# Kernel optimization log

Measured on AMD Instinct MI355X. Metric: run time of the kernel, lower is better.

## Reference

```python
import jax, jax.numpy as jnp
import numpy as np

NHEAD = 12
EPS = 1e-5


def layernorm_nobias(x, gamma):
    mu = jnp.mean(x, axis=-1, keepdims=True)
    var = jnp.var(x, axis=-1, keepdims=True)
    return (x - mu) * jax.lax.rsqrt(var + EPS) * gamma


def setup_inputs() -> dict:
    key = jax.random.key(0)
    ks = jax.random.split(key, 10)
    b, l, d = 4, 2048, 768
    s = d ** -0.5
    return {
        "x": jax.random.normal(ks[0], (b, l, d), jnp.float32),
        "Wq": jax.random.normal(ks[1], (d, d), jnp.float32) * s,
        "Wk": jax.random.normal(ks[2], (d, d), jnp.float32) * s,
        "bk": jax.random.normal(ks[3], (d,), jnp.float32) * 0.02,
        "Wv": jax.random.normal(ks[4], (d, d), jnp.float32) * s,
        "bv": jax.random.normal(ks[5], (d,), jnp.float32) * 0.02,
        "gq": jnp.ones((d,), jnp.float32),
        "gk": jnp.ones((d,), jnp.float32),
        "Wo": jax.random.normal(ks[6], (d, d), jnp.float32) * s,
        "bo": jnp.zeros((d,), jnp.float32),
    }


def reference(x, Wq, Wk, bk, Wv, bv, gq, gk, Wo, bo):
    b, l, d = x.shape
    n = NHEAD
    hd = d // n
    scale = hd ** -0.5
    # projections (torch Linear: x @ W.T + b), QK-norm over full dmodel
    q = layernorm_nobias(x @ Wq.T, gq)
    k = layernorm_nobias(x @ Wk.T + bk, gk)
    v = x @ Wv.T + bv
    # split heads: b l (n hd) -> b n l hd
    q = q.reshape(b, l, n, hd).transpose(0, 2, 1, 3)
    k = k.reshape(b, l, n, hd).transpose(0, 2, 1, 3)
    v = v.reshape(b, l, n, hd).transpose(0, 2, 1, 3)
    # scores [b, n, l_q, l_k]; NOTE: softmax over the QUERY axis (dim=-2)
    scores = jnp.einsum('bnqd,bnkd->bnqk', q, k) * scale
    attn = jax.nn.softmax(scores, axis=-2)
    o = jnp.einsum('bnqk,bnkd->bnqd', attn, v)
    o = o.transpose(0, 2, 1, 3).reshape(b, l, d)
    return o @ Wo.T + bo + x
```

## Files before the change

kernel.cpp:

```cpp
#include <hip/hip_runtime.h>
#include <cstddef>
#include <cstdint>


typedef unsigned short u16;
typedef short  bf16x8 __attribute__((ext_vector_type(8)));
typedef float  f32x4  __attribute__((ext_vector_type(4)));
typedef unsigned short u16x8 __attribute__((ext_vector_type(8)));
typedef unsigned short u16x4 __attribute__((ext_vector_type(4)));

#define B_   4
#define L_   2048
#define D_   768
#define NH_  12
#define HD_  64
#define M_   (B_*L_)
#define SC2  (0.125f * 1.44269504088896f)

__device__ __forceinline__ float ex2(float x) { return __builtin_amdgcn_exp2f(x); }

__device__ __forceinline__ u16 f2bf(float f) {
    union { float f; unsigned u; } v; v.f = f;
    unsigned r = v.u + 0x7FFFu + ((v.u >> 16) & 1u);
    return (u16)(r >> 16);
}
__device__ __forceinline__ float bf2f(u16 b) {
    union { unsigned u; float f; } v; v.u = ((unsigned)b) << 16;
    return v.f;
}
__device__ __forceinline__ unsigned fbits(float f) {
    union { float f; unsigned u; } v; v.f = f; return v.u;
}
__device__ __forceinline__ unsigned packbf(float lo, float hi) {
    return __builtin_amdgcn_perm(fbits(hi), fbits(lo), 0x07060302u);
}

__device__ __forceinline__ void gld16(const void* g, void* l) {
    __builtin_amdgcn_global_load_lds(
        (const __attribute__((address_space(1))) unsigned*)g,
        (__attribute__((address_space(3))) unsigned*)l, 16, 0, 0);
}

__global__ __launch_bounds__(256) void cvt_all(
    const float* __restrict__ X,
    const float* __restrict__ W0, const float* __restrict__ W1,
    const float* __restrict__ W2, const float* __restrict__ W3,
    u16* __restrict__ Yx,
    u16* __restrict__ Y0, u16* __restrict__ Y1,
    u16* __restrict__ Y2, u16* __restrict__ Y3)
{
    const int nX8 = (M_ * D_) / 8;
    const int nW8 = (D_ * D_) / 8;
    int i = blockIdx.x * 256 + threadIdx.x;
    if (i >= nX8 + 4 * nW8) return;
    const float* S; u16* Dst; int off;
    if (i < nX8) { S = X; Dst = Yx; off = i; }
    else {
        int j = i - nX8;
        int w = j / nW8; off = j - w * nW8;
        S   = (w == 0) ? W0 : (w == 1) ? W1 : (w == 2) ? W2 : W3;
        Dst = (w == 0) ? Y0 : (w == 1) ? Y1 : (w == 2) ? Y2 : Y3;
    }
    const float4* xp = (const float4*)S + (size_t)off * 2;
    float4 a = xp[0], b = xp[1];
    u16x8 o;
    o[0] = f2bf(a.x); o[1] = f2bf(a.y); o[2] = f2bf(a.z); o[3] = f2bf(a.w);
    o[4] = f2bf(b.x); o[5] = f2bf(b.y); o[6] = f2bf(b.z); o[7] = f2bf(b.w);
    *((u16x8*)Dst + off) = o;
}

__global__ __launch_bounds__(256, 4) void gemm_qkv(
    const u16* __restrict__ A,
    const u16* __restrict__ W0, const u16* __restrict__ W1,
    const u16* __restrict__ W2,
    const float* __restrict__ bk, const float* __restrict__ bv,
    u16* __restrict__ q_o, u16* __restrict__ k_o, u16* __restrict__ v_o)
{
    __shared__ __align__(16) u16 lds[16384];
    __shared__ float bs[128];
    const int tid  = threadIdx.x;
    const int lane = tid & 63, w = tid >> 6;
    const int s    = lane & 15, quad = lane >> 4;
    const int bid  = blockIdx.x;
    const int xcd  = bid & 7, j0 = bid >> 3;
    const int bm   = (xcd * 8 + j0 / 18) * 128;
    const int sub  = j0 % 18;
    const int seg  = sub / 6;
    const int bn   = (sub % 6) * 128;
    const u16* W = (seg == 0) ? W0 : ((seg == 1) ? W1 : W2);
    u16* OUT = (seg == 0) ? q_o : ((seg == 1) ? k_o : v_o);
    const int mh = (w >> 1) * 64, nh = (w & 1) * 64;
    const int wb = tid & ~63;
    const int cq = quad ^ ((s >> 1) & 3);

    if (tid < 128)
        bs[tid] = (seg == 1) ? bk[bn + tid] : ((seg == 2) ? bv[bn + tid] : 0.0f);

    f32x4 acc[4][4];
    #pragma unroll
    for (int j = 0; j < 4; ++j)
        #pragma unroll
        for (int i = 0; i < 4; ++i) acc[j][i] = (f32x4){0.f, 0.f, 0.f, 0.f};

    {
        int c = tid, r = c >> 2, cs = (c & 3) ^ ((r >> 1) & 3);
        gld16(A + (size_t)(bm + r) * D_ + cs * 8, lds + (size_t)wb * 8);
        gld16(W + (size_t)(bn + r) * D_ + cs * 8, lds + 8192 + (size_t)wb * 8);
        c = tid + 256; r = c >> 2; cs = (c & 3) ^ ((r >> 1) & 3);
        gld16(A + (size_t)(bm + r) * D_ + cs * 8, lds + (size_t)(wb + 256) * 8);
        gld16(W + (size_t)(bn + r) * D_ + cs * 8, lds + 8192 + (size_t)(wb + 256) * 8);
    }
    __syncthreads();

    for (int t = 0; t < 24; ++t) {
        const u16* Ab = lds + (t & 1) * 4096;
        const u16* Bb = lds + 8192 + (t & 1) * 4096;
        if (t < 23) {
            const int k0 = (t + 1) * 32;
            u16* Ad = lds + ((t + 1) & 1) * 4096;
            u16* Bd = lds + 8192 + ((t + 1) & 1) * 4096;
            int c = tid, r = c >> 2, cs = (c & 3) ^ ((r >> 1) & 3);
            gld16(A + (size_t)(bm + r) * D_ + k0 + cs * 8, Ad + (size_t)wb * 8);
            gld16(W + (size_t)(bn + r) * D_ + k0 + cs * 8, Bd + (size_t)wb * 8);
            c = tid + 256; r = c >> 2; cs = (c & 3) ^ ((r >> 1) & 3);
            gld16(A + (size_t)(bm + r) * D_ + k0 + cs * 8, Ad + (size_t)(wb + 256) * 8);
            gld16(W + (size_t)(bn + r) * D_ + k0 + cs * 8, Bd + (size_t)(wb + 256) * 8);
        }
        bf16x8 af[4], bf[4];
        #pragma unroll
        for (int i = 0; i < 4; ++i)
            af[i] = *(const bf16x8*)(Ab + (mh + i * 16 + s) * 32 + cq * 8);
        #pragma unroll
        for (int j = 0; j < 4; ++j)
            bf[j] = *(const bf16x8*)(Bb + (nh + j * 16 + s) * 32 + cq * 8);
        #pragma unroll
        for (int j = 0; j < 4; ++j)
            #pragma unroll
            for (int i = 0; i < 4; ++i)
                acc[j][i] = __builtin_amdgcn_mfma_f32_16x16x32_bf16(
                    bf[j], af[i], acc[j][i], 0, 0, 0);
        __syncthreads();
    }
    u16* Ct = lds;
    #pragma unroll
    for (int j = 0; j < 4; ++j) {
        const int n0 = nh + j * 16 + quad * 4;
        const f32x4 b4 = *(const f32x4*)(bs + n0);
        const int cn = n0 >> 3, off = n0 & 7;
        #pragma unroll
        for (int i = 0; i < 4; ++i) {
            const int m = mh + i * 16 + s;
            u16x4 ov;
            #pragma unroll
            for (int r = 0; r < 4; ++r) ov[r] = f2bf(acc[j][i][r] + b4[r]);
            *(u16x4*)(Ct + m * 128 + ((cn ^ (m & 15)) * 8) + off) = ov;
        }
    }
    __syncthreads();
    {
        const int m = tid >> 1, half = tid & 1;
        u16* dst = OUT + (size_t)(bm + m) * D_ + bn + half * 64;
        #pragma unroll
        for (int cc = 0; cc < 8; ++cc) {
            const int cn = half * 8 + cc;
            u16x8 v = *(const u16x8*)(Ct + m * 128 + ((cn ^ (m & 15)) * 8));
            *(u16x8*)(dst + cc * 8) = v;
        }
    }
}

__global__ __launch_bounds__(256, 3) void gemm_final(
    const u16* __restrict__ A, const u16* __restrict__ W,
    const float* __restrict__ bias, const float* __restrict__ resid,
    float* __restrict__ outf)
{
    __shared__ __align__(16) u16 lds[16384];
    const int tid  = threadIdx.x;
    const int lane = tid & 63, w = tid >> 6;
    const int s    = lane & 15, quad = lane >> 4;
    const int bid  = blockIdx.x;
    const int xcd  = bid & 7, j0 = bid >> 3;
    const int bm   = (xcd * 8 + j0 / 6) * 128;
    const int bn   = (j0 % 6) * 128;
    const int mh   = (w >> 1) * 64, nh = (w & 1) * 64;
    const int wb   = tid & ~63;
    const int cq   = quad ^ ((s >> 1) & 3);
    f32x4 acc[4][4];
    #pragma unroll
    for (int j = 0; j < 4; ++j)
        #pragma unroll
        for (int i = 0; i < 4; ++i) acc[j][i] = (f32x4){0.f, 0.f, 0.f, 0.f};

    {
        int c = tid, r = c >> 2, cs = (c & 3) ^ ((r >> 1) & 3);
        gld16(A + (size_t)(bm + r) * D_ + cs * 8, lds + (size_t)wb * 8);
        gld16(W + (size_t)(bn + r) * D_ + cs * 8, lds + 8192 + (size_t)wb * 8);
        c = tid + 256; r = c >> 2; cs = (c & 3) ^ ((r >> 1) & 3);
        gld16(A + (size_t)(bm + r) * D_ + cs * 8, lds + (size_t)(wb + 256) * 8);
        gld16(W + (size_t)(bn + r) * D_ + cs * 8, lds + 8192 + (size_t)(wb + 256) * 8);
    }
    __syncthreads();

    for (int t = 0; t < 24; ++t) {
        const u16* Ab = lds + (t & 1) * 4096;
        const u16* Bb = lds + 8192 + (t & 1) * 4096;
        if (t < 23) {
            const int k0 = (t + 1) * 32;
            u16* Ad = lds + ((t + 1) & 1) * 4096;
            u16* Bd = lds + 8192 + ((t + 1) & 1) * 4096;
            int c = tid, r = c >> 2, cs = (c & 3) ^ ((r >> 1) & 3);
            gld16(A + (size_t)(bm + r) * D_ + k0 + cs * 8, Ad + (size_t)wb * 8);
            gld16(W + (size_t)(bn + r) * D_ + k0 + cs * 8, Bd + (size_t)wb * 8);
            c = tid + 256; r = c >> 2; cs = (c & 3) ^ ((r >> 1) & 3);
            gld16(A + (size_t)(bm + r) * D_ + k0 + cs * 8, Ad + (size_t)(wb + 256) * 8);
            gld16(W + (size_t)(bn + r) * D_ + k0 + cs * 8, Bd + (size_t)(wb + 256) * 8);
        }
        bf16x8 af[4], bf[4];
        #pragma unroll
        for (int i = 0; i < 4; ++i)
            af[i] = *(const bf16x8*)(Ab + (mh + i * 16 + s) * 32 + cq * 8);
        #pragma unroll
        for (int j = 0; j < 4; ++j)
            bf[j] = *(const bf16x8*)(Bb + (nh + j * 16 + s) * 32 + cq * 8);
        #pragma unroll
        for (int j = 0; j < 4; ++j)
            #pragma unroll
            for (int i = 0; i < 4; ++i)
                acc[j][i] = __builtin_amdgcn_mfma_f32_16x16x32_bf16(
                    bf[j], af[i], acc[j][i], 0, 0, 0);
        __syncthreads();
    }
    #pragma unroll
    for (int j = 0; j < 4; ++j) {
        const int n0 = nh + j * 16 + quad * 4;
        const float4 b4 = *(const float4*)(bias + bn + n0);
        #pragma unroll
        for (int i = 0; i < 4; ++i) {
            const int m = mh + i * 16 + s;
            const size_t base = (size_t)(bm + m) * D_ + bn + n0;
            const float4 rs = *(const float4*)(resid + base);
            float4 o;
            o.x = acc[j][i][0] + b4.x + rs.x;
            o.y = acc[j][i][1] + b4.y + rs.y;
            o.z = acc[j][i][2] + b4.z + rs.z;
            o.w = acc[j][i][3] + b4.w + rs.w;
            *(float4*)(outf + base) = o;
        }
    }
}

__global__ __launch_bounds__(256) void ln2_bf16(
    const u16* __restrict__ Q, const u16* __restrict__ K,
    const float* __restrict__ gq, const float* __restrict__ gk,
    u16* __restrict__ Yq, u16* __restrict__ Yk)
{
    const int row = blockIdx.x;
    const int which = blockIdx.y;
    const u16* x = (which ? K : Q) + (size_t)row * D_;
    const float* gamma = which ? gk : gq;
    u16* Y = which ? Yk : Yq;
    const float scale = which ? 1.0f : (float)SC2;
    const int tid = threadIdx.x;
    float v[3];
    float lsum = 0.f, lsq = 0.f;
    #pragma unroll
    for (int e = 0; e < 3; ++e) {
        float t = bf2f(x[tid + e * 256]);
        v[e] = t; lsum += t; lsq += t * t;
    }
    #pragma unroll
    for (int off = 32; off > 0; off >>= 1) {
        lsum += __shfl_down(lsum, off);
        lsq  += __shfl_down(lsq,  off);
    }
    __shared__ float s1[4], s2[4];
    const int wv = tid >> 6, lane = tid & 63;
    if (lane == 0) { s1[wv] = lsum; s2[wv] = lsq; }
    __syncthreads();
    const float sum = s1[0] + s1[1] + s1[2] + s1[3];
    const float sq  = s2[0] + s2[1] + s2[2] + s2[3];
    const float mu  = sum * (1.0f / D_);
    const float var = sq * (1.0f / D_) - mu * mu;
    const float inv = rsqrtf(var + 1e-5f) * scale;
    #pragma unroll
    for (int e = 0; e < 3; ++e) {
        int c = tid + e * 256;
        Y[(size_t)row * D_ + c] = f2bf((v[e] - mu) * inv * gamma[c]);
    }
}

__global__ __launch_bounds__(256, 3) void attn_stats(
    const u16* __restrict__ Qb, const u16* __restrict__ Kb,
    const u16* __restrict__ Vb, u16* __restrict__ Vt)
{
    __shared__ __align__(16) u16 Ks[128 * 64];
    __shared__ __align__(16) u16 Qs[2][128 * 64];
    __shared__ float lbuf[4][64];
    __shared__ float rls[128];
    const int tid  = threadIdx.x;
    const int lane = tid & 63, w = tid >> 6;
    const int s    = lane & 15, quad = lane >> 4;
    const int s7   = s & 7;
    const int bid  = blockIdx.x;
    const int xcd  = bid & 7, j0 = bid >> 3;
    const int bh   = xcd * 6 + j0 / 16;
    const int kbase = (j0 % 16) * 128;
    const int b    = bh / NH_, h = bh % NH_;
    const u16* Qg = Qb + (size_t)b * L_ * D_ + h * HD_;
    const u16* Kg = Kb + (size_t)b * L_ * D_ + h * HD_;
    const int mh = (w >> 1) * 64;
    const int nh = (w & 1) * 64;
    const int wb = tid & ~63;

    #pragma unroll
    for (int c0 = 0; c0 < 1024; c0 += 256) {
        int c = c0 + tid, r = c >> 3, cc = (c & 7) ^ (r & 7);
        gld16(Kg + (size_t)(kbase + r) * D_ + cc * 8, Ks + (size_t)(c0 + wb) * 8);
        gld16(Qg + (size_t)r * D_ + cc * 8, Qs[0] + (size_t)(c0 + wb) * 8);
    }
    __syncthreads();
    bf16x8 kf[2][4];
    #pragma unroll
    for (int kk = 0; kk < 2; ++kk)
        #pragma unroll
        for (int i = 0; i < 4; ++i)
            kf[kk][i] = *(const bf16x8*)(Ks + (mh + i * 16 + s) * 64 +
                                         ((kk * 4 + quad) ^ s7) * 8);
    float lacc[4][4];
    #pragma unroll
    for (int i = 0; i < 4; ++i)
        #pragma unroll
        for (int r = 0; r < 4; ++r) lacc[i][r] = 0.f;

    for (int t = 0; t < 16; ++t) {
        if (t < 15) {
            const int qn = (t + 1) * 128;
            u16* Qd = Qs[(t + 1) & 1];
            #pragma unroll
            for (int c0 = 0; c0 < 1024; c0 += 256) {
                int c = c0 + tid, r = c >> 3, cc = (c & 7) ^ (r & 7);
                gld16(Qg + (size_t)(qn + r) * D_ + cc * 8, Qd + (size_t)(c0 + wb) * 8);
            }
        }
        const u16* Qt = Qs[t & 1];
        f32x4 acc[4][4];
        #pragma unroll
        for (int i = 0; i < 4; ++i)
            #pragma unroll
            for (int j = 0; j < 4; ++j) acc[i][j] = (f32x4){0.f, 0.f, 0.f, 0.f};
        #pragma unroll
        for (int kk = 0; kk < 2; ++kk) {
            bf16x8 bf[4];
            #pragma unroll
            for (int j = 0; j < 4; ++j)
                bf[j] = *(const bf16x8*)(Qt + (nh + j * 16 + s) * 64 +
                                         ((kk * 4 + quad) ^ s7) * 8);
            __builtin_amdgcn_s_setprio(1);
            #pragma unroll
            for (int i = 0; i < 4; ++i)
                #pragma unroll
                for (int j = 0; j < 4; ++j)
                    acc[i][j] = __builtin_amdgcn_mfma_f32_16x16x32_bf16(
                        kf[kk][i], bf[j], acc[i][j], 0, 0, 0);
            __builtin_amdgcn_s_setprio(0);
        }
        #pragma unroll
        for (int i = 0; i < 4; ++i)
            #pragma unroll
            for (int r = 0; r < 4; ++r) {
                float l0 = ex2(acc[i][0][r]) + ex2(acc[i][1][r]);
                float l1 = ex2(acc[i][2][r]) + ex2(acc[i][3][r]);
                lacc[i][r] += l0 + l1;
            }
        __syncthreads();
    }
    #pragma unroll
    for (int i = 0; i < 4; ++i)
        #pragma unroll
        for (int r = 0; r < 4; ++r) {
            float v = lacc[i][r];
            #pragma unroll
            for (int d2 = 1; d2 < 16; d2 <<= 1) v += __shfl_xor(v, d2);
            lacc[i][r] = v;
        }
    if (s == 0) {
        #pragma unroll
        for (int i = 0; i < 4; ++i)
            #pragma unroll
            for (int r = 0; r < 4; ++r)
                lbuf[w][i * 16 + quad * 4 + r] = lacc[i][r];
    }
    __syncthreads();
    if (tid < 128) {
        int kh = tid >> 6, kl = tid & 63;
        float l = lbuf[kh * 2][kl] + lbuf[kh * 2 + 1][kl];
        rls[tid] = 1.0f / l;
    }
    __syncthreads();

    u16 (*Ts)[72] = (u16 (*)[72])(&Qs[0][0]);
    for (int half = 0; half < 2; ++half) {
        const int l0g = kbase + half * 64;
        for (int c = tid; c < 512; c += 256) {
            int r = c >> 3, cc = c & 7;
            u16x8 val = *(const u16x8*)(Vb + (size_t)(b * L_ + l0g + r) * D_ +
                                        h * HD_ + cc * 8);
            const float rl = rls[half * 64 + r];
            #pragma unroll
            for (int e = 0; e < 8; ++e) val[e] = f2bf(bf2f(val[e]) * rl);
            *(u16x8*)(&Ts[r][cc * 8]) = val;
        }
        __syncthreads();
        const int d = tid >> 2, lc = (tid & 3) * 16;
        u16 tmp[16];
        #pragma unroll
        for (int e = 0; e < 16; ++e) tmp[e] = Ts[lc + e][d];
        u16* dst = Vt + ((size_t)bh * HD_ + d) * L_ + l0g + (lc & 32) +
                   ((lc >> 4) & 1) * 4;
        #pragma unroll
        for (int qd = 0; qd < 4; ++qd) {
            u16x4 o;
            #pragma unroll
            for (int e = 0; e < 4; ++e) o[e] = tmp[qd * 4 + e];
            *(u16x4*)(dst + qd * 8) = o;
        }
        __syncthreads();
    }
}

__global__ __launch_bounds__(256, 3) void attn_out(
    const u16* __restrict__ Qb, const u16* __restrict__ Kb,
    const u16* __restrict__ Vt, u16* __restrict__ Ob)
{
    __shared__ __align__(16) u16 Ks[3][64 * 64];
    __shared__ __align__(16) u16 Vts[3][64 * 64];
    const int tid  = threadIdx.x;
    const int lane = tid & 63, w = tid >> 6;
    const int s    = lane & 15, quad = lane >> 4;
    const int s7   = s & 7;
    const int bid  = blockIdx.x;
    const int xcd  = bid & 7, j0 = bid >> 3;
    const int bh   = xcd * 6 + j0 / 16;
    const int qbase = (j0 % 16) * 128;
    const int b    = bh / NH_, h = bh % NH_;
    const int qw   = w * 32;
    const u16* Qg = Qb + (size_t)b * L_ * D_ + h * HD_;
    const u16* Kg = Kb + (size_t)b * L_ * D_ + h * HD_;
    const u16* Vg = Vt + (size_t)bh * HD_ * L_;
    const int wb = tid & ~63;

    bf16x8 qf[2][2];
    #pragma unroll
    for (int kk = 0; kk < 2; ++kk)
        #pragma unroll
        for (int j = 0; j < 2; ++j)
            qf[kk][j] = *(const bf16x8*)(
                Qg + (size_t)(qbase + qw + j * 16 + s) * D_ + (kk * 4 + quad) * 8);

    {
        int c = tid, r = c >> 3, cc = (c & 7) ^ (r & 7);
        int c2 = tid + 256, r2 = c2 >> 3, cc2 = (c2 & 7) ^ (r2 & 7);
        gld16(Kg + (size_t)r * D_ + cc * 8,          Ks[0] + (size_t)wb * 8);
        gld16(Kg + (size_t)r2 * D_ + cc2 * 8,        Ks[0] + (size_t)(wb + 256) * 8);
        gld16(Kg + (size_t)(64 + r) * D_ + cc * 8,   Ks[1] + (size_t)wb * 8);
        gld16(Kg + (size_t)(64 + r2) * D_ + cc2 * 8, Ks[1] + (size_t)(wb + 256) * 8);
        gld16(Vg + (size_t)r * L_ + cc * 8,          Vts[0] + (size_t)wb * 8);
        gld16(Vg + (size_t)r2 * L_ + cc2 * 8,        Vts[0] + (size_t)(wb + 256) * 8);
        gld16(Vg + (size_t)r * L_ + 64 + cc * 8,     Vts[1] + (size_t)wb * 8);
        gld16(Vg + (size_t)r2 * L_ + 64 + cc2 * 8,   Vts[1] + (size_t)(wb + 256) * 8);
    }
    asm volatile("s_waitcnt vmcnt(2)" ::: "memory");
    __builtin_amdgcn_s_barrier();

    f32x4 acc_o[4][2];
    #pragma unroll
    for (int i = 0; i < 4; ++i)
        #pragma unroll
        for (int j = 0; j < 2; ++j) acc_o[i][j] = (f32x4){0.f, 0.f, 0.f, 0.f};

    f32x4 acc_s0[4][2], acc_s1[4][2];
    #pragma unroll
    for (int i = 0; i < 4; ++i)
        #pragma unroll
        for (int j = 0; j < 2; ++j) acc_s0[i][j] = (f32x4){0.f, 0.f, 0.f, 0.f};
    #pragma unroll
    for (int kk = 0; kk < 2; ++kk) {
        bf16x8 kfr[4];
        #pragma unroll
        for (int i = 0; i < 4; ++i)
            kfr[i] = *(const bf16x8*)(Ks[0] + (i * 16 + s) * 64 +
                                      ((kk * 4 + quad) ^ s7) * 8);
        #pragma unroll
        for (int i = 0; i < 4; ++i)
            #pragma unroll
            for (int j = 0; j < 2; ++j)
                acc_s0[i][j] = __builtin_amdgcn_mfma_f32_16x16x32_bf16(
                    kfr[i], qf[kk][j], acc_s0[i][j], 0, 0, 0);
    }

#define ATTN_TILE(ACCC, ACCN, TT, DO_PF, DO_S, WMODE)                          \
    do {                                                                       \
        const int t_ = (TT);                                                   \
        if (DO_PF) {                                                           \
            const int pi_ = (t_ + 2) % 3;                                      \
            const int kn_ = (t_ + 2) * 64;                                     \
            u16* Kd_ = Ks[pi_]; u16* Vd_ = Vts[pi_];                           \
            int c_ = tid, r_ = c_ >> 3, cc_ = (c_ & 7) ^ (r_ & 7);             \
            int c2_ = tid + 256, r2_ = c2_ >> 3, cc2_ = (c2_ & 7) ^ (r2_ & 7); \
            gld16(Kg + (size_t)(kn_ + r_) * D_ + cc_ * 8,                      \
                  Kd_ + (size_t)wb * 8);                                       \
            gld16(Kg + (size_t)(kn_ + r2_) * D_ + cc2_ * 8,                    \
                  Kd_ + (size_t)(wb + 256) * 8);                               \
            gld16(Vg + (size_t)r_ * L_ + kn_ + cc_ * 8,                        \
                  Vd_ + (size_t)wb * 8);                                       \
            gld16(Vg + (size_t)r2_ * L_ + kn_ + cc2_ * 8,                      \
                  Vd_ + (size_t)(wb + 256) * 8);                               \
        }                                                                      \
                 \
        unsigned pk_[4][2][2];                                                 \
        _Pragma("unroll")                                                      \
        for (int i = 0; i < 4; ++i)                                            \
            _Pragma("unroll")                                                  \
            for (int j = 0; j < 2; ++j) {                                      \
                float p0_ = ex2(ACCC[i][j][0]), p1_ = ex2(ACCC[i][j][1]);      \
                float p2_ = ex2(ACCC[i][j][2]), p3_ = ex2(ACCC[i][j][3]);      \
                pk_[i][j][0] = packbf(p0_, p1_);                               \
                pk_[i][j][1] = packbf(p2_, p3_);                               \
            }                                                                  \
        if (DO_S) {                                                            \
            const u16* Kt_ = Ks[(t_ + 1) % 3];                                 \
            _Pragma("unroll")                                                  \
            for (int i = 0; i < 4; ++i)                                        \
                _Pragma("unroll")                                              \
                for (int j = 0; j < 2; ++j)                                    \
                    ACCN[i][j] = (f32x4){0.f, 0.f, 0.f, 0.f};                  \
            _Pragma("unroll")                                                  \
            for (int kk = 0; kk < 2; ++kk) {                                   \
                bf16x8 kfr_[4];                                                \
                _Pragma("unroll")                                              \
                for (int i = 0; i < 4; ++i)                                    \
                    kfr_[i] = *(const bf16x8*)(Kt_ + (i * 16 + s) * 64 +       \
                                               ((kk * 4 + quad) ^ s7) * 8);    \
                _Pragma("unroll")                                              \
                for (int i = 0; i < 4; ++i)                                    \
                    _Pragma("unroll")                                          \
                    for (int j = 0; j < 2; ++j)                                \
                        ACCN[i][j] = __builtin_amdgcn_mfma_f32_16x16x32_bf16(  \
                            kfr_[i], qf[kk][j], ACCN[i][j], 0, 0, 0);          \
            }                                                                  \
        }                                                                      \
                                                                   \
        {                                                                      \
            const u16* Vtt_ = Vts[t_ % 3];                                     \
            _Pragma("unroll")                                                  \
            for (int kk = 0; kk < 2; ++kk) {                                   \
                bf16x8 av_[4];                                                 \
                _Pragma("unroll")                                              \
                for (int i = 0; i < 4; ++i)                                    \
                    av_[i] = *(const bf16x8*)(Vtt_ + (i * 16 + s) * 64 +       \
                                              ((kk * 4 + quad) ^ s7) * 8);     \
                __builtin_amdgcn_s_setprio(1);                                 \
                _Pragma("unroll")                                              \
                for (int j = 0; j < 2; ++j) {                                  \
                    union { unsigned u[4]; bf16x8 v; } bu_;                    \
                    bu_.u[0] = pk_[2 * kk][j][0];                              \
                    bu_.u[1] = pk_[2 * kk][j][1];                              \
                    bu_.u[2] = pk_[2 * kk + 1][j][0];                          \
                    bu_.u[3] = pk_[2 * kk + 1][j][1];                          \
                    _Pragma("unroll")                                          \
                    for (int i = 0; i < 4; ++i)                                \
                        acc_o[i][j] = __builtin_amdgcn_mfma_f32_16x16x32_bf16( \
                            av_[i], bu_.v, acc_o[i][j], 0, 0, 0);              \
                }                                                              \
                __builtin_amdgcn_s_setprio(0);                                 \
            }                                                                  \
        }                                                                      \
        if (WMODE == 2) {                                                      \
            asm volatile("s_waitcnt vmcnt(2)" ::: "memory");                   \
            __builtin_amdgcn_s_barrier();                                      \
        } else if (WMODE == 0) {                                               \
            asm volatile("s_waitcnt vmcnt(0)" ::: "memory");                   \
            __builtin_amdgcn_s_barrier();                                      \
        }                                                                      \
    } while (0)

    for (int t = 0; t < 30; t += 2) {
        ATTN_TILE(acc_s0, acc_s1, t,     1, 1, 2);
        ATTN_TILE(acc_s1, acc_s0, t + 1, 1, 1, 2);
    }
    ATTN_TILE(acc_s0, acc_s1, 30, 0, 1, 0);
    ATTN_TILE(acc_s1, acc_s0, 31, 0, 0, -1);
#undef ATTN_TILE

    __syncthreads();
    u16* Ep = (u16*)Ks;
    #pragma unroll
    for (int i = 0; i < 4; ++i) {
        const int dchunk = i * 2 + (quad >> 1), doff = (quad & 1) * 4;
        #pragma unroll
        for (int j = 0; j < 2; ++j) {
            const int q = qw + j * 16 + s;
            u16x4 ov;
            #pragma unroll
            for (int r = 0; r < 4; ++r) ov[r] = f2bf(acc_o[i][j][r]);
            *(u16x4*)(Ep + q * 64 + (dchunk ^ s7) * 8 + doff) = ov;
        }
    }
    __syncthreads();
    {
        const int q = tid >> 1, half = tid & 1, q7 = q & 7;
        u16* dst = Ob + (size_t)(b * L_ + qbase + q) * D_ + h * HD_ + half * 32;
        #pragma unroll
        for (int c = 0; c < 4; ++c) {
            const int cn = half * 4 + c;
            u16x8 v = *(const u16x8*)(Ep + q * 64 + ((cn ^ q7) * 8));
            *(u16x8*)(dst + c * 8) = v;
        }
    }
}

extern "C" void kernel_launch(void* const* d_in, const int* in_sizes, int n_in,
                              void* d_out, int out_size, void* d_ws, size_t ws_size,
                              hipStream_t stream)
{
    const float* x  = (const float*)d_in[0];
    const float* Wq = (const float*)d_in[1];
    const float* Wk = (const float*)d_in[2];
    const float* bk = (const float*)d_in[3];
    const float* Wv = (const float*)d_in[4];
    const float* bv = (const float*)d_in[5];
    const float* gq = (const float*)d_in[6];
    const float* gk = (const float*)d_in[7];
    const float* Wo = (const float*)d_in[8];
    const float* bo = (const float*)d_in[9];
    float* out = (float*)d_out;

    char* p = (char*)d_ws;
    u16* xb   = (u16*)p;  p += (size_t)M_ * D_ * 2;
    u16* qpre = (u16*)p;  p += (size_t)M_ * D_ * 2;
    u16* kpre = (u16*)p;  p += (size_t)M_ * D_ * 2;
    u16* vb   = (u16*)p;  p += (size_t)M_ * D_ * 2;
    u16* qb   = (u16*)p;  p += (size_t)M_ * D_ * 2;
    u16* kb   = (u16*)p;  p += (size_t)M_ * D_ * 2;
    u16* wqb  = (u16*)p;  p += (size_t)D_ * D_ * 2;
    u16* wkb  = (u16*)p;  p += (size_t)D_ * D_ * 2;
    u16* wvb  = (u16*)p;  p += (size_t)D_ * D_ * 2;
    u16* wob  = (u16*)p;  p += (size_t)D_ * D_ * 2;
    u16* ob = qpre;
    u16* vt = kpre;

    const int nTot8 = (M_ * D_ + 4 * D_ * D_) / 8;
    cvt_all<<<(nTot8 + 255) / 256, 256, 0, stream>>>(
        x, Wq, Wk, Wv, Wo, xb, wqb, wkb, wvb, wob);

    gemm_qkv<<<1152, 256, 0, stream>>>(
        xb, wqb, wkb, wvb, bk, bv, qpre, kpre, vb);

    ln2_bf16<<<dim3(M_, 2), 256, 0, stream>>>(qpre, kpre, gq, gk, qb, kb);

    attn_stats<<<768, 256, 0, stream>>>(qb, kb, vb, vt);
    attn_out<<<768, 256, 0, stream>>>(qb, kb, vt, ob);

    gemm_final<<<384, 256, 0, stream>>>(ob, wob, bo, x, out);
}
```

Baseline: 267.5 us.

## Vectorize layernorm rows per half-wave and triple-buffer Q tiles in attn_stats

The layernorm kernel now handles 8 rows per block, one row per 32 lanes, using 16-byte loads and stores and a shuffle-only reduction with no shared memory or block barrier. The attention-stats kernel switches from double-buffered 128-row Q tiles to triple-buffered 64-row tiles. It waits with explicit vmcnt counts so the next loads stay in flight across each barrier. This reduces LDS footprint and stall time but doubles the number of loop iterations and barriers.

Measured after the change: 270.4 us. Within noise of the previous version (+1.1%).

```diff
diff --git a/kernel.cpp b/kernel.cpp
--- a/kernel.cpp
+++ b/kernel.cpp
@@ -254,38 +254,49 @@
     const float* __restrict__ gq, const float* __restrict__ gk,
     u16* __restrict__ Yq, u16* __restrict__ Yk)
 {
-    const int row = blockIdx.x;
     const int which = blockIdx.y;
-    const u16* x = (which ? K : Q) + (size_t)row * D_;
-    const float* gamma = which ? gk : gq;
-    u16* Y = which ? Yk : Yq;
+    const int rowi  = threadIdx.x >> 5;
+    const int l32   = threadIdx.x & 31;
+    const int row   = blockIdx.x * 8 + rowi;
+    const u16* x = (which ? K : Q) + (size_t)row * D_ + l32 * 24;
+    const float* gamma = (which ? gk : gq) + l32 * 24;
+    u16* Y = (which ? Yk : Yq) + (size_t)row * D_ + l32 * 24;
     const float scale = which ? 1.0f : (float)SC2;
-    const int tid = threadIdx.x;
-    float v[3];
+
+    u16x8 vv[3];
+    float f[24];
     float lsum = 0.f, lsq = 0.f;
     #pragma unroll
     for (int e = 0; e < 3; ++e) {
-        float t = bf2f(x[tid + e * 256]);
-        v[e] = t; lsum += t; lsq += t * t;
-    }
-    #pragma unroll
-    for (int off = 32; off > 0; off >>= 1) {
-        lsum += __shfl_down(lsum, off);
-        lsq  += __shfl_down(lsq,  off);
-    }
-    __shared__ float s1[4], s2[4];
-    const int wv = tid >> 6, lane = tid & 63;
-    if (lane == 0) { s1[wv] = lsum; s2[wv] = lsq; }
-    __syncthreads();
-    const float sum = s1[0] + s1[1] + s1[2] + s1[3];
-    const float sq  = s2[0] + s2[1] + s2[2] + s2[3];
-    const float mu  = sum * (1.0f / D_);
-    const float var = sq * (1.0f / D_) - mu * mu;
+        vv[e] = *(const u16x8*)(x + e * 8);
+        #pragma unroll
+        for (int k = 0; k < 8; ++k) {
+            float t = bf2f(vv[e][k]);
+            f[e * 8 + k] = t; lsum += t; lsq += t * t;
+        }
+    }
+    #pragma unroll
+    for (int off = 16; off > 0; off >>= 1) {
+        lsum += __shfl_xor(lsum, off);
+        lsq  += __shfl_xor(lsq,  off);
+    }
+    const float mu  = lsum * (1.0f / D_);
+    const float var = lsq * (1.0f / D_) - mu * mu;
     const float inv = rsqrtf(var + 1e-5f) * scale;
     #pragma unroll
     for (int e = 0; e < 3; ++e) {
-        int c = tid + e * 256;
-        Y[(size_t)row * D_ + c] = f2bf((v[e] - mu) * inv * gamma[c]);
+        const float4 ga = *(const float4*)(gamma + e * 8);
+        const float4 gb = *(const float4*)(gamma + e * 8 + 4);
+        u16x8 o;
+        o[0] = f2bf((f[e*8+0] - mu) * inv * ga.x);
+        o[1] = f2bf((f[e*8+1] - mu) * inv * ga.y);
+        o[2] = f2bf((f[e*8+2] - mu) * inv * ga.z);
+        o[3] = f2bf((f[e*8+3] - mu) * inv * ga.w);
+        o[4] = f2bf((f[e*8+4] - mu) * inv * gb.x);
+        o[5] = f2bf((f[e*8+5] - mu) * inv * gb.y);
+        o[6] = f2bf((f[e*8+6] - mu) * inv * gb.z);
+        o[7] = f2bf((f[e*8+7] - mu) * inv * gb.w);
+        *(u16x8*)(Y + e * 8) = o;
     }
 }
 
@@ -294,7 +305,7 @@
     const u16* __restrict__ Vb, u16* __restrict__ Vt)
 {
     __shared__ __align__(16) u16 Ks[128 * 64];
-    __shared__ __align__(16) u16 Qs[2][128 * 64];
+    __shared__ __align__(16) u16 Qs[3][64 * 64];
     __shared__ float lbuf[4][64];
     __shared__ float rls[128];
     const int tid  = threadIdx.x;
@@ -309,16 +320,25 @@
     const u16* Qg = Qb + (size_t)b * L_ * D_ + h * HD_;
     const u16* Kg = Kb + (size_t)b * L_ * D_ + h * HD_;
     const int mh = (w >> 1) * 64;
-    const int nh = (w & 1) * 64;
+    const int nh = (w & 1) * 32;
     const int wb = tid & ~63;
 
-    #pragma unroll
-    for (int c0 = 0; c0 < 1024; c0 += 256) {
-        int c = c0 + tid, r = c >> 3, cc = (c & 7) ^ (r & 7);
-        gld16(Kg + (size_t)(kbase + r) * D_ + cc * 8, Ks + (size_t)(c0 + wb) * 8);
-        gld16(Qg + (size_t)r * D_ + cc * 8, Qs[0] + (size_t)(c0 + wb) * 8);
-    }
-    __syncthreads();
+    {
+        #pragma unroll
+        for (int c0 = 0; c0 < 1024; c0 += 256) {
+            int c = c0 + tid, r = c >> 3, cc = (c & 7) ^ (r & 7);
+            gld16(Kg + (size_t)(kbase + r) * D_ + cc * 8, Ks + (size_t)(c0 + wb) * 8);
+        }
+        int c = tid, r = c >> 3, cc = (c & 7) ^ (r & 7);
+        int c2 = tid + 256, r2 = c2 >> 3, cc2 = (c2 & 7) ^ (r2 & 7);
+        gld16(Qg + (size_t)r * D_ + cc * 8,          Qs[0] + (size_t)wb * 8);
+        gld16(Qg + (size_t)r2 * D_ + cc2 * 8,        Qs[0] + (size_t)(wb + 256) * 8);
+        gld16(Qg + (size_t)(64 + r) * D_ + cc * 8,   Qs[1] + (size_t)wb * 8);
+        gld16(Qg + (size_t)(64 + r2) * D_ + cc2 * 8, Qs[1] + (size_t)(wb + 256) * 8);
+    }
+    asm volatile("s_waitcnt vmcnt(2)" ::: "memory");
+    __builtin_amdgcn_s_barrier();
+
     bf16x8 kf[2][4];
     #pragma unroll
     for (int kk = 0; kk < 2; ++kk)
@@ -326,54 +346,63 @@
         for (int i = 0; i < 4; ++i)
             kf[kk][i] = *(const bf16x8*)(Ks + (mh + i * 16 + s) * 64 +
                                          ((kk * 4 + quad) ^ s7) * 8);
+    const f32x4 z4 = (f32x4){0.f, 0.f, 0.f, 0.f};
     float lacc[4][4];
     #pragma unroll
     for (int i = 0; i < 4; ++i)
         #pragma unroll
         for (int r = 0; r < 4; ++r) lacc[i][r] = 0.f;
 
-    for (int t = 0; t < 16; ++t) {
-        if (t < 15) {
-            const int qn = (t + 1) * 128;
-            u16* Qd = Qs[(t + 1) & 1];
-            #pragma unroll
-            for (int c0 = 0; c0 < 1024; c0 += 256) {
-                int c = c0 + tid, r = c >> 3, cc = (c & 7) ^ (r & 7);
-                gld16(Qg + (size_t)(qn + r) * D_ + cc * 8, Qd + (size_t)(c0 + wb) * 8);
-            }
-        }
-        const u16* Qt = Qs[t & 1];
-        f32x4 acc[4][4];
-        #pragma unroll
-        for (int i = 0; i < 4; ++i)
-            #pragma unroll
-            for (int j = 0; j < 4; ++j) acc[i][j] = (f32x4){0.f, 0.f, 0.f, 0.f};
-        #pragma unroll
-        for (int kk = 0; kk < 2; ++kk) {
-            bf16x8 bf[4];
-            #pragma unroll
-            for (int j = 0; j < 4; ++j)
-                bf[j] = *(const bf16x8*)(Qt + (nh + j * 16 + s) * 64 +
-                                         ((kk * 4 + quad) ^ s7) * 8);
+    for (int t = 0; t < 32; ++t) {
+        if (t < 30) {
+            const int qn = (t + 2) * 64;
+            u16* Qd = Qs[(t + 2) % 3];
+            int c = tid, r = c >> 3, cc = (c & 7) ^ (r & 7);
+            gld16(Qg + (size_t)(qn + r) * D_ + cc * 8, Qd + (size_t)wb * 8);
+            c = tid + 256; r = c >> 3; cc = (c & 7) ^ (r & 7);
+            gld16(Qg + (size_t)(qn + r) * D_ + cc * 8, Qd + (size_t)(wb + 256) * 8);
+        }
+        const u16* Qt = Qs[t % 3];
+        f32x4 acc[4][2];
+        {
+            bf16x8 bf[2];
+            #pragma unroll
+            for (int j = 0; j < 2; ++j)
+                bf[j] = *(const bf16x8*)(Qt + (nh + j * 16 + s) * 64 + (quad ^ s7) * 8);
             __builtin_amdgcn_s_setprio(1);
             #pragma unroll
             for (int i = 0; i < 4; ++i)
                 #pragma unroll
-                for (int j = 0; j < 4; ++j)
+                for (int j = 0; j < 2; ++j)
                     acc[i][j] = __builtin_amdgcn_mfma_f32_16x16x32_bf16(
-                        kf[kk][i], bf[j], acc[i][j], 0, 0, 0);
+                        kf[0][i], bf[j], z4, 0, 0, 0);
             __builtin_amdgcn_s_setprio(0);
+            #pragma unroll
+            for (int j = 0; j < 2; ++j)
+                bf[j] = *(const bf16x8*)(Qt + (nh + j * 16 + s) * 64 + ((4 + quad) ^ s7) * 8);
+            __builtin_amdgcn_s_setprio(1);
+            #pragma unroll
+            for (int i = 0; i < 4; ++i)
+                #pragma unroll
+                for (int j = 0; j < 2; ++j)
+                    acc[i][j] = __builtin_amdgcn_mfma_f32_16x16x32_bf16(
+                        kf[1][i], bf[j], acc[i][j], 0, 0, 0);
+            __builtin_amdgcn_s_setprio(0);
         }
         #pragma unroll
         for (int i = 0; i < 4; ++i)
             #pragma unroll
-            for (int r = 0; r < 4; ++r) {
-                float l0 = ex2(acc[i][0][r]) + ex2(acc[i][1][r]);
-                float l1 = ex2(acc[i][2][r]) + ex2(acc[i][3][r]);
-                lacc[i][r] += l0 + l1;
-            }
-        __syncthreads();
-    }
+            for (int r = 0; r < 4; ++r)
+                lacc[i][r] += ex2(acc[i][0][r]) + ex2(acc[i][1][r]);
+        if (t < 30) {
+            asm volatile("s_waitcnt vmcnt(2)" ::: "memory");
+            __builtin_amdgcn_s_barrier();
+        } else if (t == 30) {
+            asm volatile("s_waitcnt vmcnt(0)" ::: "memory");
+            __builtin_amdgcn_s_barrier();
+        }
+    }
+
     #pragma unroll
     for (int i = 0; i < 4; ++i)
         #pragma unroll
@@ -656,7 +685,7 @@
     gemm_qkv<<<1152, 256, 0, stream>>>(
         xb, wqb, wkb, wvb, bk, bv, qpre, kpre, vb);
 
-    ln2_bf16<<<dim3(M_, 2), 256, 0, stream>>>(qpre, kpre, gq, gk, qb, kb);
+    ln2_bf16<<<dim3(M_ / 8, 2), 256, 0, stream>>>(qpre, kpre, gq, gk, qb, kb);
 
     attn_stats<<<768, 256, 0, stream>>>(qb, kb, vb, vt);
     attn_out<<<768, 256, 0, stream>>>(qb, kb, vt, ob);
```

## Halve final GEMM M-tile and vectorize LayerNorm to 8 rows per block

Applied to the files above, without the earlier changes.

The final output projection GEMM now uses 64x128 tiles instead of 128x128 and launches 768 blocks instead of 384, so more work-groups can spread across the CUs. The LDS footprint shrinks and each warp keeps fewer accumulators. The QK LayerNorm kernel now processes 8 rows per 256-thread block, with 32 lanes per row using 16-byte vector loads and stores and a shuffle-only reduction, replacing a one-row-per-block kernel with shared-memory sync. The smaller GEMM tile reduces data reuse per block and adds more global loads of W.

New measurement: 270.7 us. Within noise of the previous version (+1.2%).

```diff
diff --git a/kernel.cpp b/kernel.cpp
--- a/kernel.cpp
+++ b/kernel.cpp
@@ -174,50 +174,48 @@
     const float* __restrict__ bias, const float* __restrict__ resid,
     float* __restrict__ outf)
 {
-    __shared__ __align__(16) u16 lds[16384];
+    __shared__ __align__(16) u16 lds[12288];
     const int tid  = threadIdx.x;
     const int lane = tid & 63, w = tid >> 6;
     const int s    = lane & 15, quad = lane >> 4;
     const int bid  = blockIdx.x;
     const int xcd  = bid & 7, j0 = bid >> 3;
-    const int bm   = (xcd * 8 + j0 / 6) * 128;
+    const int bm   = (xcd * 16 + j0 / 6) * 64;
     const int bn   = (j0 % 6) * 128;
-    const int mh   = (w >> 1) * 64, nh = (w & 1) * 64;
+    const int mh   = (w >> 1) * 32, nh = (w & 1) * 64;
     const int wb   = tid & ~63;
     const int cq   = quad ^ ((s >> 1) & 3);
-    f32x4 acc[4][4];
+    f32x4 acc[4][2];
     #pragma unroll
     for (int j = 0; j < 4; ++j)
         #pragma unroll
-        for (int i = 0; i < 4; ++i) acc[j][i] = (f32x4){0.f, 0.f, 0.f, 0.f};
+        for (int i = 0; i < 2; ++i) acc[j][i] = (f32x4){0.f, 0.f, 0.f, 0.f};
 
     {
         int c = tid, r = c >> 2, cs = (c & 3) ^ ((r >> 1) & 3);
         gld16(A + (size_t)(bm + r) * D_ + cs * 8, lds + (size_t)wb * 8);
-        gld16(W + (size_t)(bn + r) * D_ + cs * 8, lds + 8192 + (size_t)wb * 8);
+        gld16(W + (size_t)(bn + r) * D_ + cs * 8, lds + 4096 + (size_t)wb * 8);
         c = tid + 256; r = c >> 2; cs = (c & 3) ^ ((r >> 1) & 3);
-        gld16(A + (size_t)(bm + r) * D_ + cs * 8, lds + (size_t)(wb + 256) * 8);
-        gld16(W + (size_t)(bn + r) * D_ + cs * 8, lds + 8192 + (size_t)(wb + 256) * 8);
+        gld16(W + (size_t)(bn + r) * D_ + cs * 8, lds + 4096 + (size_t)(wb + 256) * 8);
     }
     __syncthreads();
 
     for (int t = 0; t < 24; ++t) {
-        const u16* Ab = lds + (t & 1) * 4096;
-        const u16* Bb = lds + 8192 + (t & 1) * 4096;
+        const u16* Ab = lds + (t & 1) * 2048;
+        const u16* Bb = lds + 4096 + (t & 1) * 4096;
         if (t < 23) {
             const int k0 = (t + 1) * 32;
-            u16* Ad = lds + ((t + 1) & 1) * 4096;
-            u16* Bd = lds + 8192 + ((t + 1) & 1) * 4096;
+            u16* Ad = lds + ((t + 1) & 1) * 2048;
+            u16* Bd = lds + 4096 + ((t + 1) & 1) * 4096;
             int c = tid, r = c >> 2, cs = (c & 3) ^ ((r >> 1) & 3);
             gld16(A + (size_t)(bm + r) * D_ + k0 + cs * 8, Ad + (size_t)wb * 8);
             gld16(W + (size_t)(bn + r) * D_ + k0 + cs * 8, Bd + (size_t)wb * 8);
             c = tid + 256; r = c >> 2; cs = (c & 3) ^ ((r >> 1) & 3);
-            gld16(A + (size_t)(bm + r) * D_ + k0 + cs * 8, Ad + (size_t)(wb + 256) * 8);
             gld16(W + (size_t)(bn + r) * D_ + k0 + cs * 8, Bd + (size_t)(wb + 256) * 8);
         }
-        bf16x8 af[4], bf[4];
-        #pragma unroll
-        for (int i = 0; i < 4; ++i)
+        bf16x8 af[2], bf[4];
+        #pragma unroll
+        for (int i = 0; i < 2; ++i)
             af[i] = *(const bf16x8*)(Ab + (mh + i * 16 + s) * 32 + cq * 8);
         #pragma unroll
         for (int j = 0; j < 4; ++j)
@@ -225,7 +223,7 @@
         #pragma unroll
         for (int j = 0; j < 4; ++j)
             #pragma unroll
-            for (int i = 0; i < 4; ++i)
+            for (int i = 0; i < 2; ++i)
                 acc[j][i] = __builtin_amdgcn_mfma_f32_16x16x32_bf16(
                     bf[j], af[i], acc[j][i], 0, 0, 0);
         __syncthreads();
@@ -235,7 +233,7 @@
         const int n0 = nh + j * 16 + quad * 4;
         const float4 b4 = *(const float4*)(bias + bn + n0);
         #pragma unroll
-        for (int i = 0; i < 4; ++i) {
+        for (int i = 0; i < 2; ++i) {
             const int m = mh + i * 16 + s;
             const size_t base = (size_t)(bm + m) * D_ + bn + n0;
             const float4 rs = *(const float4*)(resid + base);
@@ -254,38 +252,49 @@
     const float* __restrict__ gq, const float* __restrict__ gk,
     u16* __restrict__ Yq, u16* __restrict__ Yk)
 {
-    const int row = blockIdx.x;
     const int which = blockIdx.y;
-    const u16* x = (which ? K : Q) + (size_t)row * D_;
-    const float* gamma = which ? gk : gq;
-    u16* Y = which ? Yk : Yq;
+    const int rowi  = threadIdx.x >> 5;
+    const int l32   = threadIdx.x & 31;
+    const int row   = blockIdx.x * 8 + rowi;
+    const u16* x = (which ? K : Q) + (size_t)row * D_ + l32 * 24;
+    const float* gamma = (which ? gk : gq) + l32 * 24;
+    u16* Y = (which ? Yk : Yq) + (size_t)row * D_ + l32 * 24;
     const float scale = which ? 1.0f : (float)SC2;
-    const int tid = threadIdx.x;
-    float v[3];
+
+    u16x8 vv[3];
+    float f[24];
     float lsum = 0.f, lsq = 0.f;
     #pragma unroll
     for (int e = 0; e < 3; ++e) {
-        float t = bf2f(x[tid + e * 256]);
-        v[e] = t; lsum += t; lsq += t * t;
-    }
-    #pragma unroll
-    for (int off = 32; off > 0; off >>= 1) {
-        lsum += __shfl_down(lsum, off);
-        lsq  += __shfl_down(lsq,  off);
-    }
-    __shared__ float s1[4], s2[4];
-    const int wv = tid >> 6, lane = tid & 63;
-    if (lane == 0) { s1[wv] = lsum; s2[wv] = lsq; }
-    __syncthreads();
-    const float sum = s1[0] + s1[1] + s1[2] + s1[3];
-    const float sq  = s2[0] + s2[1] + s2[2] + s2[3];
-    const float mu  = sum * (1.0f / D_);
-    const float var = sq * (1.0f / D_) - mu * mu;
+        vv[e] = *(const u16x8*)(x + e * 8);
+        #pragma unroll
+        for (int k = 0; k < 8; ++k) {
+            float t = bf2f(vv[e][k]);
+            f[e * 8 + k] = t; lsum += t; lsq += t * t;
+        }
+    }
+    #pragma unroll
+    for (int off = 16; off > 0; off >>= 1) {
+        lsum += __shfl_xor(lsum, off);
+        lsq  += __shfl_xor(lsq,  off);
+    }
+    const float mu  = lsum * (1.0f / D_);
+    const float var = lsq * (1.0f / D_) - mu * mu;
     const float inv = rsqrtf(var + 1e-5f) * scale;
     #pragma unroll
     for (int e = 0; e < 3; ++e) {
-        int c = tid + e * 256;
-        Y[(size_t)row * D_ + c] = f2bf((v[e] - mu) * inv * gamma[c]);
+        const float4 ga = *(const float4*)(gamma + e * 8);
+        const float4 gb = *(const float4*)(gamma + e * 8 + 4);
+        u16x8 o;
+        o[0] = f2bf((f[e*8+0] - mu) * inv * ga.x);
+        o[1] = f2bf((f[e*8+1] - mu) * inv * ga.y);
+        o[2] = f2bf((f[e*8+2] - mu) * inv * ga.z);
+        o[3] = f2bf((f[e*8+3] - mu) * inv * ga.w);
+        o[4] = f2bf((f[e*8+4] - mu) * inv * gb.x);
+        o[5] = f2bf((f[e*8+5] - mu) * inv * gb.y);
+        o[6] = f2bf((f[e*8+6] - mu) * inv * gb.z);
+        o[7] = f2bf((f[e*8+7] - mu) * inv * gb.w);
+        *(u16x8*)(Y + e * 8) = o;
     }
 }
 
@@ -656,10 +665,10 @@
     gemm_qkv<<<1152, 256, 0, stream>>>(
         xb, wqb, wkb, wvb, bk, bv, qpre, kpre, vb);
 
-    ln2_bf16<<<dim3(M_, 2), 256, 0, stream>>>(qpre, kpre, gq, gk, qb, kb);
+    ln2_bf16<<<dim3(M_ / 8, 2), 256, 0, stream>>>(qpre, kpre, gq, gk, qb, kb);
 
     attn_stats<<<768, 256, 0, stream>>>(qb, kb, vb, vt);
     attn_out<<<768, 256, 0, stream>>>(qb, kb, vt, ob);
 
-    gemm_final<<<384, 256, 0, stream>>>(ob, wob, bo, x, out);
-}
+    gemm_final<<<768, 256, 0, stream>>>(ob, wob, bo, x, out);
+}
```
